# Kernel tuning notes

Hardware: AMD Instinct MI355X
Metric: run time of the kernel (lower is better)

Reference implementation:

```python
import jax, jax.numpy as jnp
import numpy as np

# Config: options = {hid_size:1280, num_lstm_layers:2, vocab_size:32000, dropout:0}
L, B, S, H, V = 2, 2, 512, 1280, 32000
C = H  # cell_size == hidden_size == input_size in BiLMEncoder(hid, hid, hid, L)


def setup_inputs() -> dict:
    key = jax.random.key(0)
    ks = jax.random.split(key, 11)
    sc = jnp.float32(0.05)
    def p(k, shape):
        return jax.random.normal(k, shape, dtype=jnp.float32) * sc
    return {
        "x": jax.random.normal(ks[0], (B, S, H), dtype=jnp.float32),
        "Wi_f": p(ks[1], (L, H, 4 * C)),   # input_linearity (no bias)
        "Ws_f": p(ks[2], (L, H, 4 * C)),   # state_linearity
        "b_f":  p(ks[3], (L, 4 * C)),      # state_linearity bias
        "Wp_f": p(ks[4], (L, C, H)),       # state_projection (no bias)
        "Wi_b": p(ks[5], (L, H, 4 * C)),
        "Ws_b": p(ks[6], (L, H, 4 * C)),
        "b_b":  p(ks[7], (L, 4 * C)),
        "Wp_b": p(ks[8], (L, C, H)),
        "W_lin": p(ks[9], (H, V)),
        "b_lin": p(ks[10], (V,)),
    }


def _lstm_dir(x, Wi, Ws, b, Wp, reverse):
    """LstmCellWithProjection over time. x: (B,S,H) -> (B,S,H)."""
    if reverse:
        x = x[:, ::-1, :]
    xp = jnp.einsum('bsh,hk->sbk', x, Wi)  # precompute input projections (S,B,4C)
    h0 = jnp.zeros((x.shape[0], H), x.dtype)
    c0 = jnp.zeros((x.shape[0], C), x.dtype)

    def step(carry, xt):
        h, c = carry
        g = xt + h @ Ws + b                      # (B,4C)
        i, f, z, o = jnp.split(g, 4, axis=-1)
        c_new = jax.nn.sigmoid(i) * jnp.tanh(z) + jax.nn.sigmoid(f) * c
        h_new = (jax.nn.sigmoid(o) * jnp.tanh(c_new)) @ Wp  # projected state
        return (h_new, c_new), h_new

    _, ys = jax.lax.scan(step, (h0, c0), xp)
    ys = jnp.transpose(ys, (1, 0, 2))  # (B,S,H)
    if reverse:
        ys = ys[:, ::-1, :]
    return ys


def _bilm(x, Wi_f, Ws_f, b_f, Wp_f, Wi_b, Ws_b, b_b, Wp_b):
    """ElmoLstm stacked bidirectional LSTM-with-projection, all-ones mask."""
    fwd_in, bwd_in = x, x
    outs = []
    for l in range(L):
        f_cache, b_cache = fwd_in, bwd_in
        f_out = _lstm_dir(fwd_in, Wi_f[l], Ws_f[l], b_f[l], Wp_f[l], reverse=False)
        b_out = _lstm_dir(bwd_in, Wi_b[l], Ws_b[l], b_b[l], Wp_b[l], reverse=True)
        if l != 0:  # residual skip between layers (ElmoLstm)
            f_out = f_out + f_cache
            b_out = b_out + b_cache
        fwd_in, bwd_in = f_out, b_out
        outs.append(jnp.concatenate([f_out, b_out], axis=-1))
    return jnp.stack(outs, axis=0)  # (L,B,S,2H)


def reference(x, Wi_f, Ws_f, b_f, Wp_f, Wi_b, Ws_b, b_b, Wp_b, W_lin, b_lin):
    enc = _bilm(x, Wi_f, Ws_f, b_f, Wp_f, Wi_b, Ws_b, b_b, Wp_b)
    fwd, bwd = enc[..., :H], enc[..., H:]
    logits_fwd = (jnp.einsum('lbsh,hv->lbsv', fwd, W_lin) + b_lin).reshape(B * S, -1)
    logits_bwd = (jnp.einsum('lbsh,hv->lbsv', bwd, W_lin) + b_lin).reshape(B * S, -1)
    return jnp.concatenate([logits_fwd, logits_bwd], axis=0)  # (2*B*S, L*V)
```

## Files before the change

### kernel.cpp

```cpp
#include <hip/hip_runtime.h>
#include <hip/hip_fp16.h>
#include <stdint.h>

#define S_LEN 512
#define HD 1280
#define GD 5120
#define VOC 32000

typedef __attribute__((ext_vector_type(8))) short short8;
typedef __attribute__((ext_vector_type(8))) _Float16 half8;
typedef __attribute__((ext_vector_type(4))) float floatx4;
typedef __attribute__((ext_vector_type(2))) _Float16 halfx2;
typedef __attribute__((ext_vector_type(4))) _Float16 halfx4;

static __device__ __forceinline__ unsigned short f2h(float f) {
  return __builtin_bit_cast(unsigned short, (_Float16)f);
}
static __device__ __forceinline__ float h2f(unsigned short h) {
  return (float)__builtin_bit_cast(_Float16, h);
}
static __device__ __forceinline__ float tanhf_fast(float x) {
  float xc = fminf(fmaxf(x, -15.f), 15.f);
  float e = __expf(2.f * xc);
  return (e - 1.f) / (e + 1.f);
}
#if __has_builtin(__builtin_amdgcn_fdot2)
static __device__ __forceinline__ float fdot2(halfx2 a, halfx2 b, float c) {
  return __builtin_amdgcn_fdot2(a, b, c, false);
}
#else
static __device__ __forceinline__ float fdot2(halfx2 a, halfx2 b, float c) {
  return c + (float)a[0]*(float)b[0] + (float)a[1]*(float)b[1];
}
#endif

__global__ __launch_bounds__(256)
void transpose_cvt(const float* __restrict__ in, unsigned short* __restrict__ out,
                   int R, int C)
{
  __shared__ float tile[32][33];
  const int c0 = blockIdx.x * 32;
  const int r0 = blockIdx.y * 32;
  const int tx = threadIdx.x & 31;
  const int ty = threadIdx.x >> 5;
#pragma unroll
  for (int p = 0; p < 4; p++) {
    int rl = ty + p * 8;
    tile[rl][tx] = in[(size_t)(r0 + rl) * C + c0 + tx];
  }
  __syncthreads();
#pragma unroll
  for (int p = 0; p < 4; p++) {
    int cl = ty + p * 8;
    out[(size_t)(c0 + cl) * R + r0 + tx] = f2h(tile[tx][cl]);
  }
}

template<int AFP32, int CMODE>
__global__ __launch_bounds__(256, 2)
void gemm_k(const void* __restrict__ Ap, const unsigned short* __restrict__ BTp,
            void* __restrict__ Cp, const float* __restrict__ bias,
            const unsigned short* __restrict__ resid,
            int M, int N, int K, int rev)
{
  __shared__ __align__(16) short As[128 * 32];
  __shared__ __align__(16) short Bs[128 * 32];
  const int tid  = threadIdx.x;
  const int row0 = blockIdx.y * 128;
  const int col0 = blockIdx.x * 128;
  const int lane = tid & 63;
  const int wid  = tid >> 6;
  const int wrow = (wid >> 1) * 64;
  const int wcol = (wid & 1) * 64;
  const int lr   = lane & 15;
  const int gg   = lane >> 4;

  floatx4 acc[4][4];
#pragma unroll
  for (int m = 0; m < 4; m++)
#pragma unroll
    for (int n = 0; n < 4; n++)
      acc[m][n] = (floatx4)0.0f;

  for (int k0 = 0; k0 < K; k0 += 32) {
    __syncthreads();
#pragma unroll
    for (int p = 0; p < 2; p++) {
      int idx = p * 256 + tid;
      int r = idx >> 2, c = idx & 3;
      short8 va;
      if constexpr (AFP32) {
        const float* src = (const float*)Ap + (size_t)(row0 + r) * K + k0 + c * 8;
        floatx4 f0 = *(const floatx4*)src;
        floatx4 f1 = *(const floatx4*)(src + 4);
        va[0] = (short)f2h(f0[0]); va[1] = (short)f2h(f0[1]);
        va[2] = (short)f2h(f0[2]); va[3] = (short)f2h(f0[3]);
        va[4] = (short)f2h(f1[0]); va[5] = (short)f2h(f1[1]);
        va[6] = (short)f2h(f1[2]); va[7] = (short)f2h(f1[3]);
      } else {
        va = *(const short8*)((const unsigned short*)Ap + (size_t)(row0 + r) * K + k0 + c * 8);
      }
      *(short8*)&As[r * 32 + ((c ^ (r & 3)) * 8)] = va;
      short8 vb = *(const short8*)(BTp + (size_t)(col0 + r) * K + k0 + c * 8);
      *(short8*)&Bs[r * 32 + ((c ^ (r & 3)) * 8)] = vb;
    }
    __syncthreads();
    short8 af[4], bfv[4];
#pragma unroll
    for (int m = 0; m < 4; m++) {
      int r = wrow + m * 16 + lr;
      af[m] = *(const short8*)&As[r * 32 + ((gg ^ (r & 3)) * 8)];
    }
#pragma unroll
    for (int n = 0; n < 4; n++) {
      int c = wcol + n * 16 + lr;
      bfv[n] = *(const short8*)&Bs[c * 32 + ((gg ^ (c & 3)) * 8)];
    }
#pragma unroll
    for (int m = 0; m < 4; m++)
#pragma unroll
      for (int n = 0; n < 4; n++)
        acc[m][n] = __builtin_amdgcn_mfma_f32_16x16x32_f16(
            __builtin_bit_cast(half8, af[m]), __builtin_bit_cast(half8, bfv[n]),
            acc[m][n], 0, 0, 0);
  }

#pragma unroll
  for (int m = 0; m < 4; m++) {
    int rbase = row0 + wrow + m * 16 + 4 * gg;
#pragma unroll
    for (int n = 0; n < 4; n++) {
      int col = col0 + wcol + n * 16 + lr;
      if constexpr (CMODE == 1) {
        halfx4 t4;
#pragma unroll
        for (int i = 0; i < 4; i++) t4[i] = (_Float16)acc[m][n][i];
        *(halfx4*)((_Float16*)Cp + (size_t)col * M + rbase) = t4;
      } else if constexpr (CMODE == 0) {
        float bv = bias[col];
#pragma unroll
        for (int i = 0; i < 4; i++) {
          int r = rbase + i;
          int b = r >> 9, s = r & 511;
          int so = rev ? (511 - s) : s;
          ((float*)Cp)[(size_t)((so << 1) | b) * GD + col] = acc[m][n][i] + bv;
        }
      } else if constexpr (CMODE == 2) {
#pragma unroll
        for (int i = 0; i < 4; i++) {
          int r = rbase + i;
          int t = r >> 1, b = r & 1;
          int s = rev ? (511 - t) : t;
          size_t o = (size_t)((b << 9) | s) * HD + col;
          float v = acc[m][n][i];
          if (resid) v += h2f(resid[o]);
          ((unsigned short*)Cp)[o] = f2h(v);
        }
      } else {
        float bv = bias[col];
#pragma unroll
        for (int i = 0; i < 4; i++)
          ((float*)Cp)[(size_t)(rbase + i) * N + col] = acc[m][n][i] + bv;
      }
    }
  }
}

__global__ __launch_bounds__(256, 1)
void lstm_scan(const _Float16* __restrict__ wfT,
               const float* __restrict__ xp,
               unsigned short* __restrict__ Pout,
               unsigned int* __restrict__ pbuf,
               unsigned int* __restrict__ ctr,
               int tbase)
{
  const int dir = blockIdx.x & 1;
  const int g   = blockIdx.x >> 1;
  const int jbase = g * 10;
  const int tid = threadIdx.x;
  const int ks  = tid & 31;
  const int cg  = tid >> 5;

  __shared__ __align__(16) unsigned int wlds[40 * 640];
  __shared__ __align__(16) unsigned int plds[1280];
  __shared__ float gvals[40][2];

#pragma unroll 1
  for (int i = 0; i < 25; i++) {
    int idx = i * 256 + tid;
    int c = idx / 160, r = idx - c * 160;
    size_t rowIdx = (size_t)dir * GD + (c / 10) * HD + jbase + (c % 10);
    const uint4* src = (const uint4*)(wfT + rowIdx * HD);
    *(uint4*)&wlds[c * 640 + r * 4] = src[r];
  }

  int gcol[5];
#pragma unroll
  for (int i = 0; i < 5; i++) {
    int c = cg * 5 + i;
    gcol[i] = (c / 10) * HD + jbase + (c % 10);
  }
  const bool isRed = (ks == 0);

  const bool isOwn = tid < 10;
  const int ob = tid & 1;
  const int op = tid >> 1;
  float cst0 = 0.f, cst1 = 0.f;

  __syncthreads();

  for (int t = 0; t < S_LEN; t++) {
    float xpv[5][2];
    if (isRed) {
#pragma unroll
      for (int i = 0; i < 5; i++)
#pragma unroll
        for (int b = 0; b < 2; b++)
          xpv[i][b] = xp[((size_t)dir * 1024 + t * 2 + b) * GD + gcol[i]];
    }

    if (t > 0) {
      if (tid < 64) {
        const unsigned tgt = (unsigned)(tbase + t) * 4u;
        const unsigned int* cp = ctr + dir * 32 + (tid & 31);
        while (true) {
          unsigned v = __hip_atomic_load(cp, __ATOMIC_RELAXED, __HIP_MEMORY_SCOPE_AGENT);
          if (__all(v >= tgt)) break;
          __builtin_amdgcn_s_sleep(1);
        }
      }
      __syncthreads();
    }

    const unsigned int* pr = pbuf + (dir * 2 + (t & 1)) * 1280;
#pragma unroll
    for (int r = 0; r < 5; r++)
      plds[r * 256 + tid] = __hip_atomic_load(pr + r * 256 + tid,
                                              __ATOMIC_RELAXED, __HIP_MEMORY_SCOPE_AGENT);
    __syncthreads();

    float acc[5][2];
#pragma unroll
    for (int i = 0; i < 5; i++) { acc[i][0] = 0.f; acc[i][1] = 0.f; }
#pragma unroll
    for (int j = 0; j < 5; j++) {
      half8 pv0 = *(const half8*)&plds[0 * 640 + ks * 20 + j * 4];
      half8 pv1 = *(const half8*)&plds[1 * 640 + ks * 20 + j * 4];
#pragma unroll
      for (int i = 0; i < 5; i++) {
        half8 wv = *(const half8*)&wlds[(cg * 5 + i) * 640 + ks * 20 + j * 4];
#pragma unroll
        for (int u = 0; u < 4; u++) {
          halfx2 w2  = {wv[2 * u], wv[2 * u + 1]};
          halfx2 p02 = {pv0[2 * u], pv0[2 * u + 1]};
          halfx2 p12 = {pv1[2 * u], pv1[2 * u + 1]};
          acc[i][0] = fdot2(p02, w2, acc[i][0]);
          acc[i][1] = fdot2(p12, w2, acc[i][1]);
        }
      }
    }

#pragma unroll
    for (int i = 0; i < 5; i++)
#pragma unroll
      for (int b = 0; b < 2; b++) {
        float v = acc[i][b];
#pragma unroll
        for (int off = 16; off >= 1; off >>= 1)
          v += __shfl_xor(v, off, 32);
        if (isRed) gvals[cg * 5 + i][b] = v + xpv[i][b];
      }
    __syncthreads();

    if (isOwn) {
      int j0 = op * 2, j1 = op * 2 + 1;
      float gi0 = gvals[j0][ob],      gi1 = gvals[j1][ob];
      float gf0 = gvals[10 + j0][ob], gf1 = gvals[10 + j1][ob];
      float gz0 = gvals[20 + j0][ob], gz1 = gvals[20 + j1][ob];
      float go0 = gvals[30 + j0][ob], go1 = gvals[30 + j1][ob];
      float si0 = 1.f / (1.f + __expf(-gi0)), si1 = 1.f / (1.f + __expf(-gi1));
      float sf0 = 1.f / (1.f + __expf(-gf0)), sf1 = 1.f / (1.f + __expf(-gf1));
      float so0 = 1.f / (1.f + __expf(-go0)), so1 = 1.f / (1.f + __expf(-go1));
      cst0 = si0 * tanhf_fast(gz0) + sf0 * cst0;
      cst1 = si1 * tanhf_fast(gz1) + sf1 * cst1;
      float pv0 = so0 * tanhf_fast(cst0);
      float pv1 = so1 * tanhf_fast(cst1);
      unsigned int packed = (unsigned)f2h(pv0) | ((unsigned)f2h(pv1) << 16);
      unsigned int* pw = pbuf + (dir * 2 + ((t + 1) & 1)) * 1280;
      __hip_atomic_store(pw + ob * 640 + (jbase >> 1) + op, packed,
                         __ATOMIC_RELAXED, __HIP_MEMORY_SCOPE_AGENT);
      ((unsigned int*)Pout)[(((size_t)dir * 1024 + t * 2 + ob) * HD + jbase) / 2 + op] = packed;
    }
    asm volatile("s_waitcnt vmcnt(0)" ::: "memory");
    if (tid == 0) {
      __hip_atomic_fetch_add(ctr + dir * 32 + (g & 31), 1u,
                             __ATOMIC_RELAXED, __HIP_MEMORY_SCOPE_AGENT);
    }
  }
}

extern "C" void kernel_launch(void* const* d_in, const int* in_sizes, int n_in,
                              void* d_out, int out_size, void* d_ws, size_t ws_size,
                              hipStream_t stream)
{
  char* W = (char*)d_ws;
  const size_t WS_T  = 0;
  const size_t WI_T  = 52428800;
  const size_t WP_T  = 104857600;
  const size_t WF_T  = 117964800;
  const size_t HCAT  = 170393600;
  const size_t P_O   = 180879360;
  const size_t XP_O  = 186122240;
  const size_t PB_O  = 228065280;
  const size_t CTR_O = 228106240;
  const size_t NEED  = 228106496;
  const size_t WLIN_T = 0;
  if (ws_size < NEED) return;

  const float* x    = (const float*)d_in[0];
  const float* Wi_f = (const float*)d_in[1];
  const float* Ws_f = (const float*)d_in[2];
  const float* b_f  = (const float*)d_in[3];
  const float* Wp_f = (const float*)d_in[4];
  const float* Wi_b = (const float*)d_in[5];
  const float* Ws_b = (const float*)d_in[6];
  const float* b_b  = (const float*)d_in[7];
  const float* Wp_b = (const float*)d_in[8];
  const float* Wlin = (const float*)d_in[9];
  const float* blin = (const float*)d_in[10];

  hipMemsetAsync(W + PB_O, 0, 40960 + 256, stream);

  for (int l = 0; l < 2; l++)
    for (int d = 0; d < 2; d++) {
      int ld = l * 2 + d;
      const float* ws_src = (d ? Ws_b : Ws_f) + (size_t)l * HD * GD;
      const float* wi_src = (d ? Wi_b : Wi_f) + (size_t)l * HD * GD;
      const float* wp_src = (d ? Wp_b : Wp_f) + (size_t)l * HD * HD;
      transpose_cvt<<<dim3(GD / 32, HD / 32), 256, 0, stream>>>(
        ws_src, (unsigned short*)(W + WS_T) + (size_t)ld * GD * HD, HD, GD);
      transpose_cvt<<<dim3(GD / 32, HD / 32), 256, 0, stream>>>(
        wi_src, (unsigned short*)(W + WI_T) + (size_t)ld * GD * HD, HD, GD);
      transpose_cvt<<<dim3(HD / 32, HD / 32), 256, 0, stream>>>(
        wp_src, (unsigned short*)(W + WP_T) + (size_t)ld * HD * HD, HD, HD);
    }

  for (int l = 0; l < 2; l++)
    for (int d = 0; d < 2; d++) {
      int ld = l * 2 + d;
      const float* wp_src = (d ? Wp_b : Wp_f) + (size_t)l * HD * HD;
      gemm_k<1, 1><<<dim3(GD / 128, HD / 128), 256, 0, stream>>>(
        wp_src, (const unsigned short*)(W + WS_T) + (size_t)ld * GD * HD,
        (void*)((_Float16*)(W + WF_T) + (size_t)ld * GD * HD),
        nullptr, nullptr, HD, GD, HD, 0);
    }

  for (int l = 0; l < 2; l++) {
    for (int d = 0; d < 2; d++) {
      int ld = l * 2 + d;
      const float* bias = (d ? b_b : b_f) + (size_t)l * GD;
      if (l == 0) {
        gemm_k<1, 0><<<dim3(GD / 128, 1024 / 128), 256, 0, stream>>>(
          x, (const unsigned short*)(W + WI_T) + (size_t)ld * GD * HD,
          (void*)((float*)(W + XP_O) + (size_t)d * 1024 * GD),
          bias, nullptr, 1024, GD, HD, d);
      } else {
        const unsigned short* Ain =
          (const unsigned short*)(W + HCAT) + (size_t)(d * 2048 + (l - 1) * 1024) * HD;
        gemm_k<0, 0><<<dim3(GD / 128, 1024 / 128), 256, 0, stream>>>(
          Ain, (const unsigned short*)(W + WI_T) + (size_t)ld * GD * HD,
          (void*)((float*)(W + XP_O) + (size_t)d * 1024 * GD),
          bias, nullptr, 1024, GD, HD, d);
      }
    }
    if (l == 1) {
      transpose_cvt<<<dim3(VOC / 32, HD / 32), 256, 0, stream>>>(
        Wlin, (unsigned short*)(W + WLIN_T), HD, VOC);
    }
    lstm_scan<<<256, 256, 0, stream>>>(
      (const _Float16*)(W + WF_T) + (size_t)l * 2 * GD * HD,
      (const float*)(W + XP_O),
      (unsigned short*)(W + P_O),
      (unsigned int*)(W + PB_O) + (size_t)l * 5120,
      (unsigned int*)(W + CTR_O),
      l * 512);
    for (int d = 0; d < 2; d++) {
      int ld = l * 2 + d;
      const unsigned short* resid = (l == 0) ? nullptr :
        (const unsigned short*)(W + HCAT) + (size_t)(d * 2048 + (l - 1) * 1024) * HD;
      gemm_k<0, 2><<<dim3(HD / 128, 1024 / 128), 256, 0, stream>>>(
        (const unsigned short*)(W + P_O) + (size_t)d * 1024 * HD,
        (const unsigned short*)(W + WP_T) + (size_t)ld * HD * HD,
        (void*)((unsigned short*)(W + HCAT) + (size_t)(d * 2048 + l * 1024) * HD),
        nullptr, resid, 1024, HD, HD, d);
    }
  }

  gemm_k<0, 3><<<dim3(VOC / 128, 4096 / 128), 256, 0, stream>>>(
    (const unsigned short*)(W + HCAT), (const unsigned short*)(W + WLIN_T),
    d_out, blin, nullptr, 4096, VOC, HD, 0);
}
```

Before: 7.256 ms.

## Replace counter-based step barrier with tagged per-element flags in LSTM scan

Cross-block synchronisation in the persistent LSTM scan no longer uses atomic counters that every block polls and increments. Each fp16 hidden value is now stored in its own 32-bit word with the timestep in the upper 16 bits, and readers spin until every word they load carries the expected tag. This removes the fence-plus-atomic-increment round trip and the separate poll-then-load phase from the serial critical path. In exchange the exchange buffer doubles in size, every thread now polls ten words instead of a few threads polling counters, and correctness depends on tag values not aliasing across layers.

```diff
diff --git a/kernel.cpp b/kernel.cpp
--- a/kernel.cpp
+++ b/kernel.cpp
@@ -171,7 +171,6 @@
                const float* __restrict__ xp,
                unsigned short* __restrict__ Pout,
                unsigned int* __restrict__ pbuf,
-               unsigned int* __restrict__ ctr,
                int tbase)
 {
   const int dir = blockIdx.x & 1;
@@ -207,6 +206,16 @@
   const int op = tid >> 1;
   float cst0 = 0.f, cst1 = 0.f;
 
+  const int pb_b = tid >> 7;
+  const int pg   = tid & 127;
+
+  if (isOwn) {
+    unsigned tag0 = ((unsigned)(unsigned short)tbase) << 16;
+    unsigned int* pw = pbuf + ((dir << 1) | 0) * 2560 + ob * 1280 + jbase + op * 2;
+    __hip_atomic_store(pw,     tag0, __ATOMIC_RELAXED, __HIP_MEMORY_SCOPE_AGENT);
+    __hip_atomic_store(pw + 1, tag0, __ATOMIC_RELAXED, __HIP_MEMORY_SCOPE_AGENT);
+  }
+
   __syncthreads();
 
   for (int t = 0; t < S_LEN; t++) {
@@ -219,24 +228,25 @@
           xpv[i][b] = xp[((size_t)dir * 1024 + t * 2 + b) * GD + gcol[i]];
     }
 
-    if (t > 0) {
-      if (tid < 64) {
-        const unsigned tgt = (unsigned)(tbase + t) * 4u;
-        const unsigned int* cp = ctr + dir * 32 + (tid & 31);
-        while (true) {
-          unsigned v = __hip_atomic_load(cp, __ATOMIC_RELAXED, __HIP_MEMORY_SCOPE_AGENT);
-          if (__all(v >= tgt)) break;
-          __builtin_amdgcn_s_sleep(1);
+    {
+      const unsigned short tagv = (unsigned short)(tbase + t);
+      const unsigned int* prw =
+        pbuf + ((dir << 1) | (t & 1)) * 2560 + pb_b * 1280 + pg * 10;
+      unsigned int wv[10];
+      for (;;) {
+        bool ok = true;
+#pragma unroll
+        for (int i = 0; i < 10; i++) {
+          wv[i] = __hip_atomic_load(prw + i, __ATOMIC_RELAXED, __HIP_MEMORY_SCOPE_AGENT);
+          ok &= ((unsigned short)(wv[i] >> 16) == tagv);
         }
-      }
-      __syncthreads();
-    }
-
-    const unsigned int* pr = pbuf + (dir * 2 + (t & 1)) * 1280;
-#pragma unroll
-    for (int r = 0; r < 5; r++)
-      plds[r * 256 + tid] = __hip_atomic_load(pr + r * 256 + tid,
-                                              __ATOMIC_RELAXED, __HIP_MEMORY_SCOPE_AGENT);
+        if (ok) break;
+        __builtin_amdgcn_s_sleep(2);
+      }
+#pragma unroll
+      for (int i = 0; i < 5; i++)
+        plds[pb_b * 640 + pg * 5 + i] = (wv[2 * i] & 0xffffu) | (wv[2 * i + 1] << 16);
+    }
     __syncthreads();
 
     float acc[5][2];
@@ -285,16 +295,15 @@
       cst1 = si1 * tanhf_fast(gz1) + sf1 * cst1;
       float pv0 = so0 * tanhf_fast(cst0);
       float pv1 = so1 * tanhf_fast(cst1);
-      unsigned int packed = (unsigned)f2h(pv0) | ((unsigned)f2h(pv1) << 16);
-      unsigned int* pw = pbuf + (dir * 2 + ((t + 1) & 1)) * 1280;
-      __hip_atomic_store(pw + ob * 640 + (jbase >> 1) + op, packed,
+      unsigned tagw = ((unsigned)(unsigned short)(tbase + t + 1)) << 16;
+      unsigned int* pw =
+        pbuf + ((dir << 1) | ((t + 1) & 1)) * 2560 + ob * 1280 + jbase + op * 2;
+      __hip_atomic_store(pw,     tagw | (unsigned)f2h(pv0),
                          __ATOMIC_RELAXED, __HIP_MEMORY_SCOPE_AGENT);
+      __hip_atomic_store(pw + 1, tagw | (unsigned)f2h(pv1),
+                         __ATOMIC_RELAXED, __HIP_MEMORY_SCOPE_AGENT);
+      unsigned packed = (unsigned)f2h(pv0) | ((unsigned)f2h(pv1) << 16);
       ((unsigned int*)Pout)[(((size_t)dir * 1024 + t * 2 + ob) * HD + jbase) / 2 + op] = packed;
-    }
-    asm volatile("s_waitcnt vmcnt(0)" ::: "memory");
-    if (tid == 0) {
-      __hip_atomic_fetch_add(ctr + dir * 32 + (g & 31), 1u,
-                             __ATOMIC_RELAXED, __HIP_MEMORY_SCOPE_AGENT);
     }
   }
 }
@@ -316,6 +325,7 @@
   const size_t NEED  = 228106496;
   const size_t WLIN_T = 0;
   if (ws_size < NEED) return;
+  (void)CTR_O;
 
   const float* x    = (const float*)d_in[0];
   const float* Wi_f = (const float*)d_in[1];
@@ -381,9 +391,8 @@
       (const _Float16*)(W + WF_T) + (size_t)l * 2 * GD * HD,
       (const float*)(W + XP_O),
       (unsigned short*)(W + P_O),
-      (unsigned int*)(W + PB_O) + (size_t)l * 5120,
-      (unsigned int*)(W + CTR_O),
-      l * 512);
+      (unsigned int*)(W + PB_O),
+      l * 1024);
     for (int d = 0; d < 2; d++) {
       int ld = l * 2 + d;
       const unsigned short* resid = (l == 0) ? nullptr :
```

New measurement: 9.901 ms. +36.5%, slower.
